# Kernel optimization log

Hardware: AMD Instinct MI355X
Metric: run time of the kernel (lower is better)

## Reference

```python
import jax, jax.numpy as jnp
import numpy as np

B, N, D, K = 4, 4096, 1024, 256
AMPLITUDE_MAX = 3.0
GATE_BIAS = float(np.log(0.65 / 0.35))  # logit(gate_bias_init=0.65)


def setup_inputs() -> dict:
    key = jax.random.key(0)
    k0, k1, k2 = jax.random.split(key, 3)
    return {
        "x": jax.random.normal(k0, (B, N, D), jnp.float32),
        "W_proj": jax.random.normal(k1, (6 * K, D), jnp.float32) * (1.0 / np.sqrt(D)),
        "b_proj": jnp.zeros((6 * K,), jnp.float32),
        "W_res": jax.random.normal(k2, (D, 2 * K), jnp.float32) * 0.002,
        "res_scale": jnp.float32(0.05),
    }


def _resonance_scan(alpha, drive_r, drive_i):
    """r_t = alpha_t * r_{t-1} + v_t, associative prefix scan over seq axis=1."""
    b = jnp.stack([drive_r, drive_i], axis=-1)      # (B, N, K, 2)
    a = alpha[..., None]                            # (B, N, K, 1)

    def combine(left, right):
        a_l, b_l = left
        a_r, b_r = right
        return (a_l * a_r, a_r * b_l + b_r)

    _, r = jax.lax.associative_scan(combine, (a, b), axis=1)
    return r[..., 0], r[..., 1]                     # (B, N, K) each


def reference(x, W_proj, b_proj, W_res, res_scale):
    n = x.shape[1]
    # OscillatorProjection: one fused linear -> 6 heads of size K
    raw = jnp.einsum('bnd,pd->bnp', x, W_proj) + b_proj        # (B, n, 6K)
    A_raw, o_raw, phi, al_raw, g_raw, be_raw = jnp.split(raw, 6, axis=-1)
    A = AMPLITUDE_MAX * jax.nn.sigmoid(A_raw)                  # amplitude in (0, amplitude_max)
    omega = jax.nn.softplus(o_raw)                             # positive frequency
    alpha = jax.nn.sigmoid(al_raw + GATE_BIAS)                 # decay gate, fp32
    g_out = jax.nn.sigmoid(g_raw)
    beta = jax.nn.sigmoid(be_raw)

    # phase_mode == 'log' positions
    pos = jnp.log1p(jnp.arange(n, dtype=jnp.float32))[None, :, None]
    angle = omega * pos + phi
    cos_a = jnp.cos(angle)
    sin_a = jnp.sin(angle)

    one_m_a = 1.0 - alpha
    drive_r = one_m_a * A * cos_a
    drive_i = one_m_a * A * sin_a

    r_r, r_i = _resonance_scan(alpha, drive_r, drive_i)

    # forget-gate erase along current phase direction
    readout = r_r * cos_a + r_i * sin_a
    r_r = r_r - beta * readout * cos_a
    r_i = r_i - beta * readout * sin_a

    # state norm: r /= max(|r|, 1.0)
    modulus = jnp.sqrt(r_r * r_r + r_i * r_i + 1e-8)
    scale = jnp.maximum(modulus, 1.0)
    r_r = r_r / scale
    r_i = r_i / scale

    # demodulate: rho = r * exp(-j*angle)
    rho_re = r_r * cos_a + r_i * sin_a
    rho_im = -r_r * sin_a + r_i * cos_a
    rho = jnp.concatenate([g_out * rho_re, g_out * rho_im], axis=-1)  # (B, n, 2K)

    # eval mode: warmup_factor = 1.0
    return res_scale * jnp.einsum('bnk,dk->bnd', rho, W_res)
```

## Files before the change

kernel.cpp:

```cpp
#include <hip/hip_runtime.h>
#include <hip/hip_bf16.h>
#include <cstdint>
#include <cstddef>

#define B_ 4
#define N_ 4096
#define D_ 1024
#define K_ 256
#define M_ (B_ * N_)
#define P_ (6 * K_)
#define DK2_ (2 * K_)

static __device__ __forceinline__ float sigm(float x) {
    return 1.0f / (1.0f + __expf(-x));
}
static __device__ __forceinline__ float softplusf_(float x) {
    return fmaxf(x, 0.0f) + __logf(1.0f + __expf(-fabsf(x)));
}
static __device__ __forceinline__ unsigned short f2bf(float f) {
    uint32_t u = __float_as_uint(f);
    uint32_t r = (u + 0x7FFFu + ((u >> 16) & 1u)) >> 16;
    return (unsigned short)r;
}

#define GATE_BIAS 0.6190392084062235f
#define AMP_MAX 3.0f

typedef __attribute__((ext_vector_type(8))) __bf16 bf16x8;
typedef __attribute__((ext_vector_type(4))) float f32x4;

static __device__ __forceinline__ void gload_lds16(const unsigned short* g, unsigned short* l) {
    __builtin_amdgcn_global_load_lds(
        (const __attribute__((address_space(1))) void*)g,
        (__attribute__((address_space(3))) void*)l, 16, 0, 0);
}

__global__ __launch_bounds__(256) void cvt_kernel(const float* __restrict__ src,
                                                  unsigned short* __restrict__ dst, int n4) {
    int i = blockIdx.x * 256 + threadIdx.x;
    if (i < n4) {
        float4 v = reinterpret_cast<const float4*>(src)[i];
        ushort4 o;
        o.x = f2bf(v.x); o.y = f2bf(v.y); o.z = f2bf(v.z); o.w = f2bf(v.w);
        reinterpret_cast<ushort4*>(dst)[i] = o;
    }
}


#define FRAG(BUF, r, kc) \
    (*reinterpret_cast<const bf16x8*>(&(BUF)[(size_t)(r) * 64 + (((((kc) >> 3) ^ ((r) & 7)) << 3))]))

template <int BN, bool ADD_BIAS, bool SCALE, typename OutT>
__global__ __launch_bounds__(512, 2) void gemm_bt(const unsigned short* __restrict__ A,
                                                  const unsigned short* __restrict__ Bm,
                                                  const float* __restrict__ bias,
                                                  const float* __restrict__ scale_p,
                                                  OutT* __restrict__ C, int M, int N, int Kd) {
    constexpr int NB = BN / 64;
    constexpr int WCOL = BN / 4;
    __shared__ unsigned short As0[256 * 64];
    __shared__ unsigned short Bs0[BN * 64];
    __shared__ unsigned short As1[256 * 64];
    __shared__ unsigned short Bs1[BN * 64];

    const int tid = threadIdx.x;
    const int w = tid >> 6, l = tid & 63;
    const int m0 = blockIdx.x * 256;
    const int n0 = blockIdx.y * BN;
    const int wm = w >> 2, wn = w & 3;
    const int lr = l & 15, lk = (l >> 4) * 8;
    const int nt = Kd >> 6;

    const int srow = tid >> 3;
    const int sslot = tid & 7;
    const int wbase = tid & ~63;

    f32x4 acc[8][NB];
#pragma unroll
    for (int mi = 0; mi < 8; ++mi)
#pragma unroll
        for (int ni = 0; ni < NB; ++ni) acc[mi][ni] = (f32x4){0.f, 0.f, 0.f, 0.f};

#define STAGE_GROUP(SRC, DST, ROW0G, K0, G)                                           \
    {                                                                                 \
        int row = (G) * 64 + srow;                                                    \
        int col = (K0) + ((sslot ^ (srow & 7)) << 3);                                 \
        gload_lds16((SRC) + (size_t)((ROW0G) + row) * Kd + col,                       \
                    (DST) + (size_t)((((G) * 512 + wbase)) * 8));                     \
    }

#define TILE_STEP(T, CA, CB, PA, PB)                                                  \
    {                                                                                 \
        const int knext = ((T) + 1) * 64;                                             \
        if ((T) + 1 < nt) {                                                           \
            _Pragma("unroll") for (int g = 0; g < 4; ++g)                             \
                STAGE_GROUP(A, PA, m0, knext, g);                                     \
            _Pragma("unroll") for (int g = 0; g < NB; ++g)                            \
                STAGE_GROUP(Bm, PB, n0, knext, g);                                    \
        }                                                                             \
        _Pragma("unroll") for (int kkI = 0; kkI < 2; ++kkI) {                         \
            const int kk = kkI * 32;                                                  \
            bf16x8 af[8], bfr[NB];                                                    \
            _Pragma("unroll") for (int f = 0; f < 8; ++f) {                           \
                int ar = wm * 128 + f * 16 + lr;                                      \
                af[f] = FRAG(CA, ar, kk + lk);                                        \
            }                                                                         \
            _Pragma("unroll") for (int f = 0; f < NB; ++f) {                          \
                int br = wn * WCOL + f * 16 + lr;                                     \
                bfr[f] = FRAG(CB, br, kk + lk);                                       \
            }                                                                         \
            _Pragma("unroll") for (int mi = 0; mi < 8; ++mi)                          \
                _Pragma("unroll") for (int ni = 0; ni < NB; ++ni)                     \
                    acc[mi][ni] = __builtin_amdgcn_mfma_f32_16x16x32_bf16(            \
                        af[mi], bfr[ni], acc[mi][ni], 0, 0, 0);                       \
        }                                                                             \
        asm volatile("s_waitcnt vmcnt(0) lgkmcnt(0)" ::: "memory");                   \
        __builtin_amdgcn_s_barrier();                                                 \
    }

#pragma unroll
    for (int g = 0; g < 4; ++g) STAGE_GROUP(A, As0, m0, 0, g);
#pragma unroll
    for (int g = 0; g < NB; ++g) STAGE_GROUP(Bm, Bs0, n0, 0, g);
    asm volatile("s_waitcnt vmcnt(0)" ::: "memory");
    __builtin_amdgcn_s_barrier();

    for (int t = 0; t < nt; t += 2) {
        TILE_STEP(t, As0, Bs0, As1, Bs1);
        TILE_STEP(t + 1, As1, Bs1, As0, Bs0);
    }

    float sc = SCALE ? *scale_p : 1.0f;
#pragma unroll
    for (int mi = 0; mi < 8; ++mi) {
        int row = m0 + wm * 128 + mi * 16 + (l >> 4) * 4;
#pragma unroll
        for (int ni = 0; ni < NB; ++ni) {
            int col = n0 + wn * WCOL + ni * 16 + lr;
            float bv = ADD_BIAS ? bias[col] : 0.0f;
#pragma unroll
            for (int j = 0; j < 4; ++j) {
                float v = acc[mi][ni][j] + bv;
                if (SCALE) v *= sc;
                C[(size_t)(row + j) * N + col] = (OutT)v;
            }
        }
    }
#undef STAGE_GROUP
#undef TILE_STEP
}

struct Step {
    float alpha, dr, di, cs, sn, g, beta;
};
template <bool FULL>
static __device__ __forceinline__ Step compute_step(const _Float16* __restrict__ p, float pos) {
    Step s;
    float a_raw = (float)p[0];
    float o_raw = (float)p[K_];
    float phi   = (float)p[2 * K_];
    float al    = (float)p[3 * K_];
    float A     = AMP_MAX * sigm(a_raw);
    float omega = softplusf_(o_raw);
    float alpha = sigm(al + GATE_BIAS);
    float angle = omega * pos + phi;
    float sn, cs;
    __sincosf(angle, &sn, &cs);
    float oma = 1.0f - alpha;
    s.alpha = alpha;
    s.dr = oma * A * cs;
    s.di = oma * A * sn;
    s.cs = cs;
    s.sn = sn;
    if (FULL) {
        s.g    = sigm((float)p[4 * K_]);
        s.beta = sigm((float)p[5 * K_]);
    }
    return s;
}

__global__ __launch_bounds__(256) void scan_sum_kernel(const _Float16* __restrict__ raw,
                                                       float* __restrict__ sA,
                                                       float* __restrict__ sR,
                                                       float* __restrict__ sI,
                                                       float* __restrict__ subA,
                                                       float* __restrict__ subR,
                                                       float* __restrict__ subI) {
    const int tid = threadIdx.x;
    const int c = tid & 15, t = tid >> 4;
    const int chunk = blockIdx.x, kg = blockIdx.y, b = blockIdx.z;
    const int k = kg * 16 + c;
    const int n0 = chunk * 256 + t * 16;
    const _Float16* base = raw + (size_t)(b * N_ + n0) * P_ + k;

    float aP = 1.0f, rR = 0.0f, rI = 0.0f;
#pragma unroll
    for (int j = 0; j < 16; ++j) {
        Step s = compute_step<false>(base + (size_t)j * P_, __logf((float)(n0 + j + 1)));
        aP *= s.alpha;
        rR = s.alpha * rR + s.dr;
        rI = s.alpha * rI + s.di;
    }
    const int chan = b * K_ + kg * 16 + c;
    const int sidx = (chunk * 16 + t) * 1024 + chan;
    subA[sidx] = aP;
    subR[sidx] = rR;
    subI[sidx] = rI;

    __shared__ float lA[256], lR[256], lI[256];
    lA[c * 16 + t] = aP;
    lR[c * 16 + t] = rR;
    lI[c * 16 + t] = rI;
    __syncthreads();
    if (tid < 16) {
        float a = 1.0f, r = 0.0f, im = 0.0f;
        for (int tt = 0; tt < 16; ++tt) {
            float at = lA[tid * 16 + tt];
            r  = at * r  + lR[tid * 16 + tt];
            im = at * im + lI[tid * 16 + tt];
            a *= at;
        }
        int chanw = b * K_ + kg * 16 + tid;
        sA[chunk * 1024 + chanw] = a;
        sR[chunk * 1024 + chanw] = r;
        sI[chunk * 1024 + chanw] = im;
    }
}

__global__ __launch_bounds__(256) void scan_apply_kernel(const _Float16* __restrict__ raw,
                                                         const float* __restrict__ sA,
                                                         const float* __restrict__ sR,
                                                         const float* __restrict__ sI,
                                                         const float* __restrict__ subA,
                                                         const float* __restrict__ subR,
                                                         const float* __restrict__ subI,
                                                         unsigned short* __restrict__ rho) {
    const int tid = threadIdx.x;
    const int c = tid & 15, t = tid >> 4;
    const int chunk = blockIdx.x, kg = blockIdx.y, b = blockIdx.z;
    const int k = kg * 16 + c;
    const int n0 = chunk * 256 + t * 16;
    const _Float16* base = raw + (size_t)(b * N_ + n0) * P_ + k;

    float pR = 0.0f, pI = 0.0f;
    if (tid < 16) {
        int chan = b * K_ + kg * 16 + tid;
        for (int ch = 0; ch < chunk; ++ch) {
            float a = sA[ch * 1024 + chan];
            pR = a * pR + sR[ch * 1024 + chan];
            pI = a * pI + sI[ch * 1024 + chan];
        }
    }
    __shared__ float lA[256], lR[256], lI[256], pTR[256], pTI[256];
    {
        const int chan = b * K_ + kg * 16 + c;
        const int sidx = (chunk * 16 + t) * 1024 + chan;
        lA[c * 16 + t] = subA[sidx];
        lR[c * 16 + t] = subR[sidx];
        lI[c * 16 + t] = subI[sidx];
    }
    __syncthreads();
    if (tid < 16) {
        float r = pR, im = pI;
        for (int tt = 0; tt < 16; ++tt) {
            pTR[tid * 16 + tt] = r;
            pTI[tid * 16 + tt] = im;
            float at = lA[tid * 16 + tt];
            r  = at * r  + lR[tid * 16 + tt];
            im = at * im + lI[tid * 16 + tt];
        }
    }
    __syncthreads();
    float r = pTR[c * 16 + t], im = pTI[c * 16 + t];
    unsigned short* orow = rho + (size_t)(b * N_ + n0) * DK2_ + k;
#pragma unroll
    for (int j = 0; j < 16; ++j) {
        Step s = compute_step<true>(base + (size_t)j * P_, __logf((float)(n0 + j + 1)));
        r  = s.alpha * r  + s.dr;
        im = s.alpha * im + s.di;
        float readout = r * s.cs + im * s.sn;
        float r2 = r  - s.beta * readout * s.cs;
        float i3 = im - s.beta * readout * s.sn;
        float mod = __fsqrt_rn(r2 * r2 + i3 * i3 + 1e-8f);
        float scl = fmaxf(mod, 1.0f);
        float inv = 1.0f / scl;
        float rr = r2 * inv, ri = i3 * inv;
        float rho_re = rr * s.cs + ri * s.sn;
        float rho_im = -rr * s.sn + ri * s.cs;
        orow[(size_t)j * DK2_]      = f2bf(s.g * rho_re);
        orow[(size_t)j * DK2_ + K_] = f2bf(s.g * rho_im);
    }
}

extern "C" void kernel_launch(void* const* d_in, const int* in_sizes, int n_in,
                              void* d_out, int out_size, void* d_ws, size_t ws_size,
                              hipStream_t stream) {
    const float* x  = (const float*)d_in[0];
    const float* Wp = (const float*)d_in[1];
    const float* bp = (const float*)d_in[2];
    const float* Wr = (const float*)d_in[3];
    const float* rs = (const float*)d_in[4];
    float* out = (float*)d_out;
    char* ws = (char*)d_ws;

    _Float16* raw = (_Float16*)ws;
    unsigned short* xb  = (unsigned short*)(ws + 100663296);
    unsigned short* wpb = (unsigned short*)(ws + 134217728);
    unsigned short* wrb = (unsigned short*)(ws + 137363456);
    float* sA = (float*)(ws + 138412032);
    float* sR = (float*)(ws + 138477568);
    float* sI = (float*)(ws + 138543104);
    unsigned short* rho = xb;
    float* subA = (float*)(ws + 134217728);
    float* subR = (float*)(ws + 135266304);
    float* subI = (float*)(ws + 136314880);

    cvt_kernel<<<16384, 256, 0, stream>>>(x, xb, M_ * D_ / 4);
    cvt_kernel<<<1536, 256, 0, stream>>>(Wp, wpb, P_ * D_ / 4);
    cvt_kernel<<<512, 256, 0, stream>>>(Wr, wrb, D_ * DK2_ / 4);

    gemm_bt<192, true, false, _Float16><<<dim3(M_ / 256, P_ / 192), 512, 0, stream>>>(
        xb, wpb, bp, nullptr, raw, M_, P_, D_);

    scan_sum_kernel<<<dim3(16, 16, 4), 256, 0, stream>>>(raw, sA, sR, sI, subA, subR, subI);
    scan_apply_kernel<<<dim3(16, 16, 4), 256, 0, stream>>>(raw, sA, sR, sI, subA, subR, subI, rho);

    gemm_bt<256, false, true, float><<<dim3(M_ / 256, D_ / 256), 512, 0, stream>>>(
        rho, wrb, nullptr, rs, out, M_, D_, DK2_);
}
```

Measured before the change: 142.6 us.

## Software-pipeline LDS fragment loads with MFMAs in projection GEMM

```diff
diff --git a/kernel.cpp b/kernel.cpp
--- a/kernel.cpp
+++ b/kernel.cpp
@@ -50,7 +50,7 @@
 #define FRAG(BUF, r, kc) \
     (*reinterpret_cast<const bf16x8*>(&(BUF)[(size_t)(r) * 64 + (((((kc) >> 3) ^ ((r) & 7)) << 3))]))
 
-template <int BN, bool ADD_BIAS, bool SCALE, typename OutT>
+template <int BN, bool PIPE, bool ADD_BIAS, bool SCALE, typename OutT>
 __global__ __launch_bounds__(512, 2) void gemm_bt(const unsigned short* __restrict__ A,
                                                   const unsigned short* __restrict__ Bm,
                                                   const float* __restrict__ bias,
@@ -89,45 +89,81 @@
                     (DST) + (size_t)((((G) * 512 + wbase)) * 8));                     \
     }
 
+#define STAGE_ALL(PA, PB, K0)                                                         \
+    {                                                                                 \
+        _Pragma("unroll") for (int g = 0; g < 4; ++g)                                 \
+            STAGE_GROUP(A, PA, m0, K0, g);                                            \
+        _Pragma("unroll") for (int g = 0; g < NB; ++g)                                \
+            STAGE_GROUP(Bm, PB, n0, K0, g);                                           \
+    }
+
+#define RLOAD(DA, DB, CA, CB, KK)                                                     \
+    {                                                                                 \
+        _Pragma("unroll") for (int f = 0; f < 8; ++f) {                               \
+            int ar = wm * 128 + f * 16 + lr;                                          \
+            DA[f] = FRAG(CA, ar, (KK) + lk);                                          \
+        }                                                                             \
+        _Pragma("unroll") for (int f = 0; f < NB; ++f) {                              \
+            int br = wn * WCOL + f * 16 + lr;                                         \
+            DB[f] = FRAG(CB, br, (KK) + lk);                                          \
+        }                                                                             \
+    }
+
+#define MFMAS(SA, SB)                                                                 \
+    {                                                                                 \
+        __builtin_amdgcn_s_setprio(1);                                                \
+        _Pragma("unroll") for (int mi = 0; mi < 8; ++mi)                              \
+            _Pragma("unroll") for (int ni = 0; ni < NB; ++ni)                         \
+                acc[mi][ni] = __builtin_amdgcn_mfma_f32_16x16x32_bf16(                \
+                    SA[mi], SB[ni], acc[mi][ni], 0, 0, 0);                            \
+        __builtin_amdgcn_s_setprio(0);                                                \
+    }
+
+#define WAITS_BARRIER                                                                 \
+    asm volatile("s_waitcnt vmcnt(0) lgkmcnt(0)" ::: "memory");                       \
+    __builtin_amdgcn_s_barrier();
+
+    if constexpr (PIPE) {
+        bf16x8 afX[8], bfrX[NB], afY[8], bfrY[NB];
+        STAGE_ALL(As0, Bs0, 0);
+        asm volatile("s_waitcnt vmcnt(0)" ::: "memory");
+        __builtin_amdgcn_s_barrier();
+        RLOAD(afX, bfrX, As0, Bs0, 0);
+
+        for (int t = 0; t < nt; t += 2) {
+            STAGE_ALL(As1, Bs1, (t + 1) * 64);
+            RLOAD(afY, bfrY, As0, Bs0, 32);
+            MFMAS(afX, bfrX);
+            WAITS_BARRIER;
+            RLOAD(afX, bfrX, As1, Bs1, 0);
+            MFMAS(afY, bfrY);
+            if (t + 2 < nt) STAGE_ALL(As0, Bs0, (t + 2) * 64);
+            RLOAD(afY, bfrY, As1, Bs1, 32);
+            MFMAS(afX, bfrX);
+            WAITS_BARRIER;
+            if (t + 2 < nt) RLOAD(afX, bfrX, As0, Bs0, 0);
+            MFMAS(afY, bfrY);
+        }
+    } else {
 #define TILE_STEP(T, CA, CB, PA, PB)                                                  \
     {                                                                                 \
-        const int knext = ((T) + 1) * 64;                                             \
-        if ((T) + 1 < nt) {                                                           \
-            _Pragma("unroll") for (int g = 0; g < 4; ++g)                             \
-                STAGE_GROUP(A, PA, m0, knext, g);                                     \
-            _Pragma("unroll") for (int g = 0; g < NB; ++g)                            \
-                STAGE_GROUP(Bm, PB, n0, knext, g);                                    \
-        }                                                                             \
+        if ((T) + 1 < nt) STAGE_ALL(PA, PB, ((T) + 1) * 64);                          \
         _Pragma("unroll") for (int kkI = 0; kkI < 2; ++kkI) {                         \
             const int kk = kkI * 32;                                                  \
             bf16x8 af[8], bfr[NB];                                                    \
-            _Pragma("unroll") for (int f = 0; f < 8; ++f) {                           \
-                int ar = wm * 128 + f * 16 + lr;                                      \
-                af[f] = FRAG(CA, ar, kk + lk);                                        \
-            }                                                                         \
-            _Pragma("unroll") for (int f = 0; f < NB; ++f) {                          \
-                int br = wn * WCOL + f * 16 + lr;                                     \
-                bfr[f] = FRAG(CB, br, kk + lk);                                       \
-            }                                                                         \
-            _Pragma("unroll") for (int mi = 0; mi < 8; ++mi)                          \
-                _Pragma("unroll") for (int ni = 0; ni < NB; ++ni)                     \
-                    acc[mi][ni] = __builtin_amdgcn_mfma_f32_16x16x32_bf16(            \
-                        af[mi], bfr[ni], acc[mi][ni], 0, 0, 0);                       \
+            RLOAD(af, bfr, CA, CB, kk);                                               \
+            MFMAS(af, bfr);                                                           \
         }                                                                             \
-        asm volatile("s_waitcnt vmcnt(0) lgkmcnt(0)" ::: "memory");                   \
-        __builtin_amdgcn_s_barrier();                                                 \
-    }
-
-#pragma unroll
-    for (int g = 0; g < 4; ++g) STAGE_GROUP(A, As0, m0, 0, g);
-#pragma unroll
-    for (int g = 0; g < NB; ++g) STAGE_GROUP(Bm, Bs0, n0, 0, g);
-    asm volatile("s_waitcnt vmcnt(0)" ::: "memory");
-    __builtin_amdgcn_s_barrier();
-
-    for (int t = 0; t < nt; t += 2) {
-        TILE_STEP(t, As0, Bs0, As1, Bs1);
-        TILE_STEP(t + 1, As1, Bs1, As0, Bs0);
+        WAITS_BARRIER;                                                                \
+    }
+        STAGE_ALL(As0, Bs0, 0);
+        asm volatile("s_waitcnt vmcnt(0)" ::: "memory");
+        __builtin_amdgcn_s_barrier();
+        for (int t = 0; t < nt; t += 2) {
+            TILE_STEP(t, As0, Bs0, As1, Bs1);
+            TILE_STEP(t + 1, As1, Bs1, As0, Bs0);
+        }
+#undef TILE_STEP
     }
 
     float sc = SCALE ? *scale_p : 1.0f;
@@ -147,7 +183,10 @@
         }
     }
 #undef STAGE_GROUP
-#undef TILE_STEP
+#undef STAGE_ALL
+#undef RLOAD
+#undef MFMAS
+#undef WAITS_BARRIER
 }
 
 struct Step {
@@ -319,12 +358,12 @@
     cvt_kernel<<<1536, 256, 0, stream>>>(Wp, wpb, P_ * D_ / 4);
     cvt_kernel<<<512, 256, 0, stream>>>(Wr, wrb, D_ * DK2_ / 4);
 
-    gemm_bt<192, true, false, _Float16><<<dim3(M_ / 256, P_ / 192), 512, 0, stream>>>(
+    gemm_bt<192, true, true, false, _Float16><<<dim3(M_ / 256, P_ / 192), 512, 0, stream>>>(
         xb, wpb, bp, nullptr, raw, M_, P_, D_);
 
     scan_sum_kernel<<<dim3(16, 16, 4), 256, 0, stream>>>(raw, sA, sR, sI, subA, subR, subI);
     scan_apply_kernel<<<dim3(16, 16, 4), 256, 0, stream>>>(raw, sA, sR, sI, subA, subR, subI, rho);
 
-    gemm_bt<256, false, true, float><<<dim3(M_ / 256, D_ / 256), 512, 0, stream>>>(
+    gemm_bt<256, false, false, true, float><<<dim3(M_ / 256, D_ / 256), 512, 0, stream>>>(
         rho, wrb, nullptr, rs, out, M_, D_, DK2_);
 }
```

New measurement: 143.3 us. Within noise of the previous version (+0.4%).

## Halve GEMM K-tile to 32, templatize M tile, raise occupancy, add MFMA priority

Applied to the files above, without the earlier changes.

```diff
diff --git a/kernel.cpp b/kernel.cpp
--- a/kernel.cpp
+++ b/kernel.cpp
@@ -47,81 +47,87 @@
 }
 
 
-#define FRAG(BUF, r, kc) \
-    (*reinterpret_cast<const bf16x8*>(&(BUF)[(size_t)(r) * 64 + (((((kc) >> 3) ^ ((r) & 7)) << 3))]))
-
-template <int BN, bool ADD_BIAS, bool SCALE, typename OutT>
-__global__ __launch_bounds__(512, 2) void gemm_bt(const unsigned short* __restrict__ A,
+#define FRAG32(BUF, r, ks) \
+    (*reinterpret_cast<const bf16x8*>(&(BUF)[(size_t)(r) * 32 + ((((ks) ^ (((r) >> 1) & 3))) << 3)]))
+
+template <int BM, int BN, bool ADD_BIAS, bool SCALE, typename OutT>
+__global__ __launch_bounds__(512, 4) void gemm_bt(const unsigned short* __restrict__ A,
                                                   const unsigned short* __restrict__ Bm,
                                                   const float* __restrict__ bias,
                                                   const float* __restrict__ scale_p,
                                                   OutT* __restrict__ C, int M, int N, int Kd) {
-    constexpr int NB = BN / 64;
+    constexpr int MR = BM / 32;
+    constexpr int NBF = BN / 64;
     constexpr int WCOL = BN / 4;
-    __shared__ unsigned short As0[256 * 64];
-    __shared__ unsigned short Bs0[BN * 64];
-    __shared__ unsigned short As1[256 * 64];
-    __shared__ unsigned short Bs1[BN * 64];
+    __shared__ unsigned short As0[BM * 32];
+    __shared__ unsigned short Bs0[BN * 32];
+    __shared__ unsigned short As1[BM * 32];
+    __shared__ unsigned short Bs1[BN * 32];
 
     const int tid = threadIdx.x;
     const int w = tid >> 6, l = tid & 63;
-    const int m0 = blockIdx.x * 256;
+    const int m0 = blockIdx.x * BM;
     const int n0 = blockIdx.y * BN;
     const int wm = w >> 2, wn = w & 3;
-    const int lr = l & 15, lk = (l >> 4) * 8;
-    const int nt = Kd >> 6;
-
-    const int srow = tid >> 3;
-    const int sslot = tid & 7;
-    const int wbase = tid & ~63;
-
-    f32x4 acc[8][NB];
-#pragma unroll
-    for (int mi = 0; mi < 8; ++mi)
-#pragma unroll
-        for (int ni = 0; ni < NB; ++ni) acc[mi][ni] = (f32x4){0.f, 0.f, 0.f, 0.f};
-
-#define STAGE_GROUP(SRC, DST, ROW0G, K0, G)                                           \
+    const int lr = l & 15;
+    const int ks = l >> 4;
+    const int nt = Kd >> 5;
+
+    const int srow = tid >> 2;
+    const int sslot = tid & 3;
+    const int wbase8 = (tid & ~63) * 8;
+
+    f32x4 acc[MR][NBF];
+#pragma unroll
+    for (int mi = 0; mi < MR; ++mi)
+#pragma unroll
+        for (int ni = 0; ni < NBF; ++ni) acc[mi][ni] = (f32x4){0.f, 0.f, 0.f, 0.f};
+
+#define STAGE_ALL(PA, PB, K0)                                                         \
     {                                                                                 \
-        int row = (G) * 64 + srow;                                                    \
-        int col = (K0) + ((sslot ^ (srow & 7)) << 3);                                 \
-        gload_lds16((SRC) + (size_t)((ROW0G) + row) * Kd + col,                       \
-                    (DST) + (size_t)((((G) * 512 + wbase)) * 8));                     \
+        _Pragma("unroll") for (int g = 0; g < BM / 128; ++g) {                        \
+            int row = g * 128 + srow;                                                 \
+            int col = (K0) + ((sslot ^ ((row >> 1) & 3)) << 3);                       \
+            gload_lds16(A + (size_t)(m0 + row) * Kd + col, (PA) + g * 4096 + wbase8); \
+        }                                                                             \
+        _Pragma("unroll") for (int g = 0; g < BN / 128; ++g) {                        \
+            int row = g * 128 + srow;                                                 \
+            int col = (K0) + ((sslot ^ ((row >> 1) & 3)) << 3);                       \
+            gload_lds16(Bm + (size_t)(n0 + row) * Kd + col, (PB) + g * 4096 + wbase8);\
+        }                                                                             \
+        if constexpr ((BN % 128) != 0) {                                              \
+            if (tid < 256) {                                                          \
+                int row = (BN / 128) * 128 + srow;                                    \
+                int col = (K0) + ((sslot ^ ((row >> 1) & 3)) << 3);                   \
+                gload_lds16(Bm + (size_t)(n0 + row) * Kd + col,                       \
+                            (PB) + (BN / 128) * 4096 + wbase8);                       \
+            }                                                                         \
+        }                                                                             \
     }
 
 #define TILE_STEP(T, CA, CB, PA, PB)                                                  \
     {                                                                                 \
-        const int knext = ((T) + 1) * 64;                                             \
-        if ((T) + 1 < nt) {                                                           \
-            _Pragma("unroll") for (int g = 0; g < 4; ++g)                             \
-                STAGE_GROUP(A, PA, m0, knext, g);                                     \
-            _Pragma("unroll") for (int g = 0; g < NB; ++g)                            \
-                STAGE_GROUP(Bm, PB, n0, knext, g);                                    \
-        }                                                                             \
-        _Pragma("unroll") for (int kkI = 0; kkI < 2; ++kkI) {                         \
-            const int kk = kkI * 32;                                                  \
-            bf16x8 af[8], bfr[NB];                                                    \
-            _Pragma("unroll") for (int f = 0; f < 8; ++f) {                           \
-                int ar = wm * 128 + f * 16 + lr;                                      \
-                af[f] = FRAG(CA, ar, kk + lk);                                        \
-            }                                                                         \
-            _Pragma("unroll") for (int f = 0; f < NB; ++f) {                          \
-                int br = wn * WCOL + f * 16 + lr;                                     \
-                bfr[f] = FRAG(CB, br, kk + lk);                                       \
-            }                                                                         \
-            _Pragma("unroll") for (int mi = 0; mi < 8; ++mi)                          \
-                _Pragma("unroll") for (int ni = 0; ni < NB; ++ni)                     \
-                    acc[mi][ni] = __builtin_amdgcn_mfma_f32_16x16x32_bf16(            \
-                        af[mi], bfr[ni], acc[mi][ni], 0, 0, 0);                       \
-        }                                                                             \
+        if ((T) + 1 < nt) STAGE_ALL(PA, PB, ((T) + 1) * 32);                          \
+        bf16x8 af[MR], bfr[NBF];                                                      \
+        _Pragma("unroll") for (int f = 0; f < MR; ++f) {                              \
+            int ar = wm * (BM / 2) + f * 16 + lr;                                     \
+            af[f] = FRAG32(CA, ar, ks);                                               \
+        }                                                                             \
+        _Pragma("unroll") for (int f = 0; f < NBF; ++f) {                             \
+            int br = wn * WCOL + f * 16 + lr;                                         \
+            bfr[f] = FRAG32(CB, br, ks);                                              \
+        }                                                                             \
+        __builtin_amdgcn_s_setprio(1);                                                \
+        _Pragma("unroll") for (int mi = 0; mi < MR; ++mi)                             \
+            _Pragma("unroll") for (int ni = 0; ni < NBF; ++ni)                        \
+                acc[mi][ni] = __builtin_amdgcn_mfma_f32_16x16x32_bf16(                \
+                    af[mi], bfr[ni], acc[mi][ni], 0, 0, 0);                           \
+        __builtin_amdgcn_s_setprio(0);                                                \
         asm volatile("s_waitcnt vmcnt(0) lgkmcnt(0)" ::: "memory");                   \
         __builtin_amdgcn_s_barrier();                                                 \
     }
 
-#pragma unroll
-    for (int g = 0; g < 4; ++g) STAGE_GROUP(A, As0, m0, 0, g);
-#pragma unroll
-    for (int g = 0; g < NB; ++g) STAGE_GROUP(Bm, Bs0, n0, 0, g);
+    STAGE_ALL(As0, Bs0, 0);
     asm volatile("s_waitcnt vmcnt(0)" ::: "memory");
     __builtin_amdgcn_s_barrier();
 
@@ -132,10 +138,10 @@
 
     float sc = SCALE ? *scale_p : 1.0f;
 #pragma unroll
-    for (int mi = 0; mi < 8; ++mi) {
-        int row = m0 + wm * 128 + mi * 16 + (l >> 4) * 4;
-#pragma unroll
-        for (int ni = 0; ni < NB; ++ni) {
+    for (int mi = 0; mi < MR; ++mi) {
+        int row = m0 + wm * (BM / 2) + mi * 16 + (l >> 4) * 4;
+#pragma unroll
+        for (int ni = 0; ni < NBF; ++ni) {
             int col = n0 + wn * WCOL + ni * 16 + lr;
             float bv = ADD_BIAS ? bias[col] : 0.0f;
 #pragma unroll
@@ -146,7 +152,7 @@
             }
         }
     }
-#undef STAGE_GROUP
+#undef STAGE_ALL
 #undef TILE_STEP
 }
 
@@ -319,12 +325,12 @@
     cvt_kernel<<<1536, 256, 0, stream>>>(Wp, wpb, P_ * D_ / 4);
     cvt_kernel<<<512, 256, 0, stream>>>(Wr, wrb, D_ * DK2_ / 4);
 
-    gemm_bt<192, true, false, _Float16><<<dim3(M_ / 256, P_ / 192), 512, 0, stream>>>(
+    gemm_bt<256, 192, true, false, _Float16><<<dim3(M_ / 256, P_ / 192), 512, 0, stream>>>(
         xb, wpb, bp, nullptr, raw, M_, P_, D_);
 
     scan_sum_kernel<<<dim3(16, 16, 4), 256, 0, stream>>>(raw, sA, sR, sI, subA, subR, subI);
     scan_apply_kernel<<<dim3(16, 16, 4), 256, 0, stream>>>(raw, sA, sR, sI, subA, subR, subI, rho);
 
-    gemm_bt<256, false, true, float><<<dim3(M_ / 256, D_ / 256), 512, 0, stream>>>(
+    gemm_bt<128, 128, false, true, float><<<dim3(M_ / 128, D_ / 128), 512, 0, stream>>>(
         rho, wrb, nullptr, rs, out, M_, D_, DK2_);
 }
```

Result: slower. 331.5 us (+132.4%).

## Fuse fp32-to-bf16 conversion of x into the projection GEMM A-tile load

Applied to the files above, without the earlier changes.

```diff
diff --git a/kernel.cpp b/kernel.cpp
--- a/kernel.cpp
+++ b/kernel.cpp
@@ -21,6 +21,9 @@
     uint32_t u = __float_as_uint(f);
     uint32_t r = (u + 0x7FFFu + ((u >> 16) & 1u)) >> 16;
     return (unsigned short)r;
+}
+static __device__ __forceinline__ uint32_t pk2bf(float lo, float hi) {
+    return (uint32_t)f2bf(lo) | ((uint32_t)f2bf(hi) << 16);
 }
 
 #define GATE_BIAS 0.6190392084062235f
@@ -50,8 +53,9 @@
 #define FRAG(BUF, r, kc) \
     (*reinterpret_cast<const bf16x8*>(&(BUF)[(size_t)(r) * 64 + (((((kc) >> 3) ^ ((r) & 7)) << 3))]))
 
-template <int BN, bool ADD_BIAS, bool SCALE, typename OutT>
+template <int BN, bool CVTA, bool ADD_BIAS, bool SCALE, typename OutT>
 __global__ __launch_bounds__(512, 2) void gemm_bt(const unsigned short* __restrict__ A,
+                                                  const float* __restrict__ Af,
                                                   const unsigned short* __restrict__ Bm,
                                                   const float* __restrict__ bias,
                                                   const float* __restrict__ scale_p,
@@ -74,6 +78,7 @@
     const int srow = tid >> 3;
     const int sslot = tid & 7;
     const int wbase = tid & ~63;
+    const int acol = (sslot ^ (srow & 7)) << 3;
 
     f32x4 acc[8][NB];
 #pragma unroll
@@ -81,22 +86,51 @@
 #pragma unroll
         for (int ni = 0; ni < NB; ++ni) acc[mi][ni] = (f32x4){0.f, 0.f, 0.f, 0.f};
 
-#define STAGE_GROUP(SRC, DST, ROW0G, K0, G)                                           \
-    {                                                                                 \
-        int row = (G) * 64 + srow;                                                    \
-        int col = (K0) + ((sslot ^ (srow & 7)) << 3);                                 \
-        gload_lds16((SRC) + (size_t)((ROW0G) + row) * Kd + col,                       \
-                    (DST) + (size_t)((((G) * 512 + wbase)) * 8));                     \
+#define A_GLOAD(PA, K0)                                                               \
+    {                                                                                 \
+        _Pragma("unroll") for (int g = 0; g < 4; ++g) {                               \
+            int row = g * 64 + srow;                                                  \
+            gload_lds16(A + (size_t)(m0 + row) * Kd + (K0) + acol,                    \
+                        (PA) + ((g * 512 + wbase)) * 8);                              \
+        }                                                                             \
+    }
+#define A_ISSUE(K0)                                                                   \
+    {                                                                                 \
+        _Pragma("unroll") for (int g = 0; g < 4; ++g) {                               \
+            const float4* p = reinterpret_cast<const float4*>(                        \
+                Af + (size_t)(m0 + g * 64 + srow) * Kd + (K0) + acol);                \
+            av[g][0] = p[0];                                                          \
+            av[g][1] = p[1];                                                          \
+        }                                                                             \
+    }
+#define A_WRITE(PA)                                                                   \
+    {                                                                                 \
+        _Pragma("unroll") for (int g = 0; g < 4; ++g) {                               \
+            int4 wv;                                                                  \
+            wv.x = (int)pk2bf(av[g][0].x, av[g][0].y);                                \
+            wv.y = (int)pk2bf(av[g][0].z, av[g][0].w);                                \
+            wv.z = (int)pk2bf(av[g][1].x, av[g][1].y);                                \
+            wv.w = (int)pk2bf(av[g][1].z, av[g][1].w);                                \
+            *reinterpret_cast<int4*>(&(PA)[(size_t)g * 4096 + tid * 8]) = wv;         \
+        }                                                                             \
+    }
+#define B_GLOAD(PB, K0)                                                               \
+    {                                                                                 \
+        _Pragma("unroll") for (int g = 0; g < NB; ++g) {                              \
+            int row = g * 64 + srow;                                                  \
+            gload_lds16(Bm + (size_t)(n0 + row) * Kd + (K0) + acol,                   \
+                        (PB) + ((g * 512 + wbase)) * 8);                              \
+        }                                                                             \
     }
 
 #define TILE_STEP(T, CA, CB, PA, PB)                                                  \
     {                                                                                 \
         const int knext = ((T) + 1) * 64;                                             \
-        if ((T) + 1 < nt) {                                                           \
-            _Pragma("unroll") for (int g = 0; g < 4; ++g)                             \
-                STAGE_GROUP(A, PA, m0, knext, g);                                     \
-            _Pragma("unroll") for (int g = 0; g < NB; ++g)                            \
-                STAGE_GROUP(Bm, PB, n0, knext, g);                                    \
+        const bool ds = ((T) + 1 < nt);                                               \
+        float4 av[4][2];                                                              \
+        if (ds) {                                                                     \
+            if constexpr (CVTA) { A_ISSUE(knext); } else { A_GLOAD(PA, knext); }      \
+            B_GLOAD(PB, knext);                                                       \
         }                                                                             \
         _Pragma("unroll") for (int kkI = 0; kkI < 2; ++kkI) {                         \
             const int kk = kkI * 32;                                                  \
@@ -109,21 +143,32 @@
                 int br = wn * WCOL + f * 16 + lr;                                     \
                 bfr[f] = FRAG(CB, br, kk + lk);                                       \
             }                                                                         \
+            __builtin_amdgcn_s_setprio(1);                                            \
             _Pragma("unroll") for (int mi = 0; mi < 8; ++mi)                          \
                 _Pragma("unroll") for (int ni = 0; ni < NB; ++ni)                     \
                     acc[mi][ni] = __builtin_amdgcn_mfma_f32_16x16x32_bf16(            \
                         af[mi], bfr[ni], acc[mi][ni], 0, 0, 0);                       \
+            __builtin_amdgcn_s_setprio(0);                                            \
+        }                                                                             \
+        if (ds) {                                                                     \
+            if constexpr (CVTA) { A_WRITE(PA); }                                      \
         }                                                                             \
         asm volatile("s_waitcnt vmcnt(0) lgkmcnt(0)" ::: "memory");                   \
         __builtin_amdgcn_s_barrier();                                                 \
     }
 
-#pragma unroll
-    for (int g = 0; g < 4; ++g) STAGE_GROUP(A, As0, m0, 0, g);
-#pragma unroll
-    for (int g = 0; g < NB; ++g) STAGE_GROUP(Bm, Bs0, n0, 0, g);
-    asm volatile("s_waitcnt vmcnt(0)" ::: "memory");
-    __builtin_amdgcn_s_barrier();
+    {
+        float4 av[4][2];
+        if constexpr (CVTA) {
+            A_ISSUE(0);
+            A_WRITE(As0);
+        } else {
+            A_GLOAD(As0, 0);
+        }
+        B_GLOAD(Bs0, 0);
+        asm volatile("s_waitcnt vmcnt(0) lgkmcnt(0)" ::: "memory");
+        __builtin_amdgcn_s_barrier();
+    }
 
     for (int t = 0; t < nt; t += 2) {
         TILE_STEP(t, As0, Bs0, As1, Bs1);
@@ -146,7 +191,10 @@
             }
         }
     }
-#undef STAGE_GROUP
+#undef A_GLOAD
+#undef A_ISSUE
+#undef A_WRITE
+#undef B_GLOAD
 #undef TILE_STEP
 }
 
@@ -304,27 +352,25 @@
     char* ws = (char*)d_ws;
 
     _Float16* raw = (_Float16*)ws;
-    unsigned short* xb  = (unsigned short*)(ws + 100663296);
-    unsigned short* wpb = (unsigned short*)(ws + 134217728);
+    unsigned short* rho = (unsigned short*)(ws + 100663296);
+    unsigned short* wpb = (unsigned short*)(ws + 134217728 - 4194304);
     unsigned short* wrb = (unsigned short*)(ws + 137363456);
     float* sA = (float*)(ws + 138412032);
     float* sR = (float*)(ws + 138477568);
     float* sI = (float*)(ws + 138543104);
-    unsigned short* rho = xb;
-    float* subA = (float*)(ws + 134217728);
-    float* subR = (float*)(ws + 135266304);
-    float* subI = (float*)(ws + 136314880);
-
-    cvt_kernel<<<16384, 256, 0, stream>>>(x, xb, M_ * D_ / 4);
+    float* subA = (float*)(ws + 119537664);
+    float* subR = (float*)(ws + 120586240);
+    float* subI = (float*)(ws + 121634816);
+
     cvt_kernel<<<1536, 256, 0, stream>>>(Wp, wpb, P_ * D_ / 4);
     cvt_kernel<<<512, 256, 0, stream>>>(Wr, wrb, D_ * DK2_ / 4);
 
-    gemm_bt<192, true, false, _Float16><<<dim3(M_ / 256, P_ / 192), 512, 0, stream>>>(
-        xb, wpb, bp, nullptr, raw, M_, P_, D_);
+    gemm_bt<192, true, true, false, _Float16><<<dim3(M_ / 256, P_ / 192), 512, 0, stream>>>(
+        nullptr, x, wpb, bp, nullptr, raw, M_, P_, D_);
 
     scan_sum_kernel<<<dim3(16, 16, 4), 256, 0, stream>>>(raw, sA, sR, sI, subA, subR, subI);
     scan_apply_kernel<<<dim3(16, 16, 4), 256, 0, stream>>>(raw, sA, sR, sI, subA, subR, subI, rho);
 
-    gemm_bt<256, false, true, float><<<dim3(M_ / 256, D_ / 256), 512, 0, stream>>>(
-        rho, wrb, nullptr, rs, out, M_, D_, DK2_);
-}
+    gemm_bt<256, false, false, true, float><<<dim3(M_ / 256, D_ / 256), 512, 0, stream>>>(
+        rho, nullptr, wrb, nullptr, rs, out, M_, D_, DK2_);
+}
```

After: 285.3 us. 2x slower.
